# Optimization experiments

Measured on AMD Instinct MI355X. Metric: run time of the kernel, lower is better.

## Reference

```python
import jax, jax.numpy as jnp
import numpy as np

N = 100000   # node_size
R = 1000     # rel_size
T = 600000   # triple_size (edges)
D = 128      # node_dim
DEPTH = 2


def seg_softmax(logits, seg, num_segments):
    # softmax over irregular segments (rows of a sparse [N,N] matrix)
    m = jax.lax.stop_gradient(jax.ops.segment_max(logits, seg, num_segments=num_segments))
    e = jnp.exp(logits - m[seg])
    s = jax.ops.segment_sum(e, seg, num_segments=num_segments)
    return e / s[seg]


def setup_inputs() -> dict:
    key = jax.random.key(0)
    ks = jax.random.split(key, 10)
    xav = float(np.sqrt(6.0 / (D + 1)))
    features = jax.random.normal(ks[0], (N, D), dtype=jnp.float32)
    rel_emb = jax.random.normal(ks[1], (R, D), dtype=jnp.float32)
    # adj: (2, T) COO edges; rows sorted to mimic coalesced sparse tensor
    adj_row = jnp.sort(jax.random.randint(ks[2], (T,), 0, N))
    adj_col = jax.random.randint(ks[3], (T,), 0, N)
    adj = jnp.stack([adj_row, adj_col]).astype(jnp.int64)
    # r_index: (2, T) indices of sparse [T, R] matrix, one relation per triple
    r_index = jnp.stack([jnp.arange(T), jax.random.randint(ks[4], (T,), 0, R)]).astype(jnp.int64)
    r_val = jax.random.uniform(ks[5], (T,), dtype=jnp.float32)
    hn_row = jnp.sort(jax.random.randint(ks[6], (T,), 0, N))
    hn_col = jax.random.randint(ks[7], (T,), 0, N)
    high_nei = jnp.stack([hn_row, hn_col]).astype(jnp.int64)
    attn_kernels = jax.random.uniform(ks[8], (DEPTH, D, 1), jnp.float32, -xav, xav)
    high_atts = jax.random.uniform(ks[9], (DEPTH, D, 1), jnp.float32, -xav, xav)
    return {"features": features, "rel_emb": rel_emb, "r_val": r_val,
            "attn_kernels": attn_kernels, "high_atts": high_atts,
            "adj": adj, "r_index": r_index, "high_nei": high_nei}


def reference(features, rel_emb, r_val, attn_kernels, high_atts, adj, r_index, high_nei):
    row, col = adj[0], adj[1]
    hrow, hcol = high_nei[0], high_nei[1]
    outputs = []
    feats = jnp.tanh(features)
    outputs.append(feats)
    for l in range(DEPTH):
        # sparse [T,R] @ rel_emb -> per-triple relation embedding [T,D]
        tri_rel = jax.ops.segment_sum(r_val[:, None] * rel_emb[r_index[1]],
                                      r_index[0], num_segments=T)
        tri_rel = tri_rel / jnp.maximum(
            jnp.linalg.norm(tri_rel, axis=1, keepdims=True), 1e-12)
        neighs = feats[col]                                   # [T,D] gather
        # Householder reflection of neighbor features across tri_rel
        neighs = neighs - 2.0 * jnp.sum(neighs * tri_rel, axis=1, keepdims=True) * tri_rel
        att = (tri_rel @ attn_kernels[l])[:, 0]               # [T]
        att = seg_softmax(att, row, N)                        # sparse row softmax
        feats = jnp.tanh(jax.ops.segment_sum(neighs * att[:, None], row, num_segments=N))
        outputs.append(feats)
    for l in range(DEPTH):
        neighs = feats[hcol]                                  # [T,D]
        att = seg_softmax((neighs @ high_atts[l])[:, 0], hrow, N)
        feats = jnp.tanh(jax.ops.segment_sum(neighs * att[:, None], hrow, num_segments=N))
        outputs.append(feats)
    return jnp.concatenate(outputs, axis=-1)                  # [N, D*(2*DEPTH+1)]
```

## Files before the change

### kernel.cpp

```cpp
#include <hip/hip_runtime.h>
#include <math.h>

#define N_NODES 100000
#define R_REL   1000
#define T_TRI   600000
#define D_DIM   128
#define OUT_STRIDE 640

typedef unsigned int  u32;
typedef unsigned short u16;

__device__ __forceinline__ float wave_sum(float v) {
    #pragma unroll
    for (int off = 32; off > 0; off >>= 1) v += __shfl_xor(v, off);
    return v;
}
__device__ __forceinline__ float half32_sum(float v) {
    v += __shfl_xor(v, 1); v += __shfl_xor(v, 2); v += __shfl_xor(v, 4);
    v += __shfl_xor(v, 8); v += __shfl_xor(v, 16);
    return v;
}
__device__ __forceinline__ float sub16_sum(float v) {
    v += __shfl_xor(v, 1); v += __shfl_xor(v, 2);
    v += __shfl_xor(v, 4); v += __shfl_xor(v, 8);
    return v;
}
__device__ __forceinline__ float fast_tanh(float x) {
    float e = __expf(2.f * x);
    return 1.f - __fdividef(2.f, e + 1.f);
}
__device__ __forceinline__ float4 tanh4(float4 v) {
    float4 o; o.x = fast_tanh(v.x); o.y = fast_tanh(v.y);
    o.z = fast_tanh(v.z); o.w = fast_tanh(v.w);
    return o;
}
__device__ __forceinline__ float dot4(float4 a, float4 b) {
    return a.x*b.x + a.y*b.y + a.z*b.z + a.w*b.w;
}
__device__ __forceinline__ u32 bfr(float x) {
    u32 u = __float_as_uint(x);
    return (u + 0x7fffu + ((u >> 16) & 1u)) >> 16;
}
__device__ __forceinline__ uint2 pack_bf4(float4 v) {
    uint2 p;
    p.x = bfr(v.x) | (bfr(v.y) << 16);
    p.y = bfr(v.z) | (bfr(v.w) << 16);
    return p;
}
__device__ __forceinline__ void unpack_bf8(uint4 v, float f[8]) {
    f[0] = __uint_as_float(v.x << 16); f[1] = __uint_as_float(v.x & 0xffff0000u);
    f[2] = __uint_as_float(v.y << 16); f[3] = __uint_as_float(v.y & 0xffff0000u);
    f[4] = __uint_as_float(v.z << 16); f[5] = __uint_as_float(v.z & 0xffff0000u);
    f[6] = __uint_as_float(v.w << 16); f[7] = __uint_as_float(v.w & 0xffff0000u);
}

__global__ void k_tanh(const float* __restrict__ feat, float* __restrict__ out,
                       u16* __restrict__ bf0) {
    int i = blockIdx.x * blockDim.x + threadIdx.x;
    if (i >= N_NODES * D_DIM / 4) return;
    int n  = i / (D_DIM / 4);
    int d4 = i % (D_DIM / 4);
    float4 v = reinterpret_cast<const float4*>(feat)[i];
    float4 t = tanh4(v);
    reinterpret_cast<float4*>(out + (size_t)n * OUT_STRIDE)[d4] = t;
    reinterpret_cast<uint2*>(bf0 + (size_t)n * D_DIM)[d4] = pack_bf4(t);
}

__global__ void k_relprep(const float* __restrict__ rel, const float* __restrict__ attk,
                          float* __restrict__ wtab, float* __restrict__ fsc) {
    int r = blockIdx.x;
    int lane = threadIdx.x;
    float a0 = rel[r * D_DIM + lane], a1 = rel[r * D_DIM + 64 + lane];
    float nrm2 = wave_sum(a0 * a0 + a1 * a1);
    float d0  = wave_sum(a0 * attk[lane] + a1 * attk[64 + lane]);
    float d1  = wave_sum(a0 * attk[D_DIM + lane] + a1 * attk[D_DIM + 64 + lane]);
    if (lane == 0) {
        float inv = __frsqrt_rn(nrm2);
        wtab[r]         = __expf(d0 * inv);
        wtab[R_REL + r] = __expf(d1 * inv);
        fsc[r] = 2.f * inv * inv;
    }
}

__global__ void k_pack_rel(const float* __restrict__ rel, u16* __restrict__ relbf) {
    int t = blockIdx.x * blockDim.x + threadIdx.x;
    if (t >= R_REL * 16) return;
    int r = t >> 4, k = t & 15;
    const float4* src = (const float4*)(rel + (size_t)r * D_DIM + k * 8);
    uint2 pa = pack_bf4(src[0]), pb = pack_bf4(src[1]);
    uint4 o; o.x = pa.x; o.y = pa.y; o.z = pb.x; o.w = pb.y;
    ((uint4*)(relbf + (size_t)r * D_DIM))[k] = o;
}

__global__ void k_rowptr2(const int* __restrict__ rows_a, const int* __restrict__ rows_b,
                          int* __restrict__ pa, int* __restrict__ pb) {
    int i = blockIdx.x * blockDim.x + threadIdx.x;
    const int* rows; int* p; int n;
    if (i <= N_NODES) { rows = rows_a; p = pa; n = i; }
    else {
        n = i - (N_NODES + 1);
        if (n > N_NODES) return;
        rows = rows_b; p = pb;
    }
    int lo = 0, hi = T_TRI;
    while (lo < hi) { int mid = (lo + hi) >> 1; if (rows[mid] < n) lo = mid + 1; else hi = mid; }
    p[n] = lo;
}

__global__ __launch_bounds__(256) void k_nr_layer(
    float* __restrict__ outbuf, int out_off,
    const u16* __restrict__ in_bf,
    u16* __restrict__ out_bf,
    const int* __restrict__ row_ptr,
    const int* __restrict__ col,
    const int* __restrict__ ridx1,
    const float* __restrict__ r_val,
    const u16* __restrict__ rel_bf,
    const float* __restrict__ wtab,
    const float* __restrict__ fsc,
    const float* __restrict__ ha,
    float* __restrict__ eproj_out) {
    __shared__ float s_w[4][64];
    __shared__ float s_fs[4][64];
    int wslot = threadIdx.x >> 6;
    int lane  = threadIdx.x & 63;
    int wid2  = (blockIdx.x * blockDim.x + threadIdx.x) >> 6;
    int row   = wid2 * 2 + (lane >> 5);
    if (row >= N_NODES) return;
    int ll  = lane & 31;
    int sgl = (lane >> 4) & 1;
    int sl  = lane & 15;
    int beg = row_ptr[row], end = row_ptr[row + 1];
    int deg = end - beg;
    float* orow = outbuf + (size_t)row * OUT_STRIDE + out_off;

    if (deg == 0) {
        float4 z = {0.f,0.f,0.f,0.f};
        ((float4*)orow)[ll] = z;
        if (out_bf != nullptr && ll < 16) {
            uint4 zz = {0u,0u,0u,0u};
            ((uint4*)(out_bf + (size_t)row * D_DIM))[ll] = zz;
        }
        if (ha != nullptr && ll == 0) eproj_out[row] = 1.f;
        return;
    }

    int  t0 = beg + ll;
    bool va = t0 < end;
    int  ta = va ? t0 : beg;
    int  rt_a = ridx1[ta];
    float rv_a = r_val[ta];
    bool  z_a  = (rv_a == 0.f);
    float w_a  = z_a ? 1.f : wtab[rt_a];
    float fs_a = z_a ? 0.f : fsc[rt_a];
    w_a = va ? w_a : 0.f;

    int  tb0 = beg + sgl, tb1 = beg + 2 + sgl;
    bool v0 = tb0 < end, v1 = tb1 < end;
    int  tc0 = v0 ? tb0 : beg, tc1 = v1 ? tb1 : beg;
    int  cc0 = col[tc0],   cc1 = col[tc1];
    int  rr0 = ridx1[tc0], rr1 = ridx1[tc1];
    uint4 F0 = ((const uint4*)(in_bf  + (size_t)cc0 * D_DIM))[sl];
    uint4 R0 = ((const uint4*)(rel_bf + (size_t)rr0 * D_DIM))[sl];
    uint4 F1 = ((const uint4*)(in_bf  + (size_t)cc1 * D_DIM))[sl];
    uint4 R1 = ((const uint4*)(rel_bf + (size_t)rr1 * D_DIM))[sl];

    float lsum = w_a;
    for (int t = t0 + 32; t < end; t += 32) {
        int rt = ridx1[t]; float rv = r_val[t];
        lsum += (rv == 0.f) ? 1.f : wtab[rt];
    }
    float inv_s = 1.f / half32_sum(lsum);
    s_w[wslot][lane]  = w_a * inv_s;
    s_fs[wslot][lane] = fs_a;

    int hb = lane & 32;

    float w0  = v0 ? s_w[wslot][hb + sgl] : 0.f;
    float fs0 = s_fs[wslot][hb + sgl];
    float nf[8], rf[8];
    unpack_bf8(F0, nf); unpack_bf8(R0, rf);
    float pd = 0.f;
    #pragma unroll
    for (int j = 0; j < 8; ++j) pd += nf[j] * rf[j];
    pd = sub16_sum(pd);
    float f0 = fs0 * pd;
    float acc[8];
    #pragma unroll
    for (int j = 0; j < 8; ++j) acc[j] = w0 * (nf[j] - f0 * rf[j]);

    int niter = (deg + 1) >> 1;
    int cur_tc = tc1, cur_rr = rr1; bool cur_v = v1;
    for (int it = 1; it < niter; ++it) {
        int tb = beg + 2 * (it + 1) + sgl;
        bool nv = tb < end;
        int  ntc = nv ? tb : beg;
        int  ncc = col[ntc];
        int  nrr = ridx1[ntc];
        uint4 NF = ((const uint4*)(in_bf  + (size_t)ncc * D_DIM))[sl];
        uint4 NR = ((const uint4*)(rel_bf + (size_t)nrr * D_DIM))[sl];

        int idx = 2 * it + sgl;
        float w, fs;
        if (idx < 32) {
            w  = cur_v ? s_w[wslot][hb + idx] : 0.f;
            fs = s_fs[wslot][hb + idx];
        } else {
            float rv = r_val[cur_tc];
            bool z = (rv == 0.f);
            w  = cur_v ? (z ? 1.f : wtab[cur_rr]) * inv_s : 0.f;
            fs = z ? 0.f : fsc[cur_rr];
        }
        float gf[8], qf[8];
        unpack_bf8(F1, gf); unpack_bf8(R1, qf);
        float pdt = 0.f;
        #pragma unroll
        for (int j = 0; j < 8; ++j) pdt += gf[j] * qf[j];
        pdt = sub16_sum(pdt);
        float ft = fs * pdt;
        #pragma unroll
        for (int j = 0; j < 8; ++j) acc[j] += w * (gf[j] - ft * qf[j]);

        F1 = NF; R1 = NR;
        cur_tc = ntc; cur_rr = nrr; cur_v = nv;
    }

    #pragma unroll
    for (int j = 0; j < 8; ++j) acc[j] += __shfl_xor(acc[j], 16);

    float4 q = (sgl == 0) ? make_float4(acc[0], acc[1], acc[2], acc[3])
                          : make_float4(acc[4], acc[5], acc[6], acc[7]);
    float4 tq = tanh4(q);
    ((float4*)orow)[2 * sl + sgl] = tq;
    if (out_bf != nullptr)
        ((uint2*)(out_bf + (size_t)row * D_DIM))[2 * sl + sgl] = pack_bf4(tq);
    if (ha != nullptr) {
        const float4* ha4 = (const float4*)ha;
        float pdp = dot4(tq, ha4[2 * sl + sgl]);
        pdp = sub16_sum(pdp);
        pdp += __shfl_xor(pdp, 16);
        if (ll == 0) eproj_out[row] = __expf(pdp);
    }
}

__global__ __launch_bounds__(256) void k_high_layer(
    float* __restrict__ outbuf, int out_off,
    const u16* __restrict__ in_bf,
    u16* __restrict__ out_bf,
    const int* __restrict__ row_ptr,
    const int* __restrict__ hcol,
    const float* __restrict__ eproj,
    const float* __restrict__ ha,
    float* __restrict__ eproj_out) {
    __shared__ float s_w[4][64];
    int wslot = threadIdx.x >> 6;
    int lane  = threadIdx.x & 63;
    int wid2  = (blockIdx.x * blockDim.x + threadIdx.x) >> 6;
    int row   = wid2 * 2 + (lane >> 5);
    if (row >= N_NODES) return;
    int ll  = lane & 31;
    int sgl = (lane >> 4) & 1;
    int sl  = lane & 15;
    int beg = row_ptr[row], end = row_ptr[row + 1];
    int deg = end - beg;
    float* orow = outbuf + (size_t)row * OUT_STRIDE + out_off;

    if (deg == 0) {
        float4 z = {0.f,0.f,0.f,0.f};
        ((float4*)orow)[ll] = z;
        if (out_bf != nullptr && ll < 16) {
            uint4 zz = {0u,0u,0u,0u};
            ((uint4*)(out_bf + (size_t)row * D_DIM))[ll] = zz;
        }
        if (ha != nullptr && ll == 0) eproj_out[row] = 1.f;
        return;
    }

    int  t0 = beg + ll;
    bool va = t0 < end;
    int  ta = va ? t0 : beg;
    int  c_a = hcol[ta];
    float e_a = eproj[c_a];
    e_a = va ? e_a : 0.f;

    int  tb0 = beg + sgl, tb1 = beg + 2 + sgl;
    bool v0 = tb0 < end, v1 = tb1 < end;
    int  tc0 = v0 ? tb0 : beg, tc1 = v1 ? tb1 : beg;
    int  cc0 = hcol[tc0], cc1 = hcol[tc1];
    uint4 F0 = ((const uint4*)(in_bf + (size_t)cc0 * D_DIM))[sl];
    uint4 F1 = ((const uint4*)(in_bf + (size_t)cc1 * D_DIM))[sl];

    float lsum = e_a;
    for (int t = t0 + 32; t < end; t += 32)
        lsum += eproj[hcol[t]];
    float inv_s = 1.f / half32_sum(lsum);
    s_w[wslot][lane] = e_a * inv_s;

    int hb = lane & 32;

    float w0 = v0 ? s_w[wslot][hb + sgl] : 0.f;
    float nf[8];
    unpack_bf8(F0, nf);
    float acc[8];
    #pragma unroll
    for (int j = 0; j < 8; ++j) acc[j] = w0 * nf[j];

    int niter = (deg + 1) >> 1;
    int cur_cc = cc1; bool cur_v = v1;
    for (int it = 1; it < niter; ++it) {
        int tb = beg + 2 * (it + 1) + sgl;
        bool nv = tb < end;
        int  ntc = nv ? tb : beg;
        int  ncc = hcol[ntc];
        uint4 NF = ((const uint4*)(in_bf + (size_t)ncc * D_DIM))[sl];

        int idx = 2 * it + sgl;
        float w;
        if (idx < 32) w = cur_v ? s_w[wslot][hb + idx] : 0.f;
        else          w = cur_v ? eproj[cur_cc] * inv_s : 0.f;
        float gf[8];
        unpack_bf8(F1, gf);
        #pragma unroll
        for (int j = 0; j < 8; ++j) acc[j] += w * gf[j];

        F1 = NF; cur_cc = ncc; cur_v = nv;
    }

    #pragma unroll
    for (int j = 0; j < 8; ++j) acc[j] += __shfl_xor(acc[j], 16);

    float4 q = (sgl == 0) ? make_float4(acc[0], acc[1], acc[2], acc[3])
                          : make_float4(acc[4], acc[5], acc[6], acc[7]);
    float4 tq = tanh4(q);
    ((float4*)orow)[2 * sl + sgl] = tq;
    if (out_bf != nullptr)
        ((uint2*)(out_bf + (size_t)row * D_DIM))[2 * sl + sgl] = pack_bf4(tq);
    if (ha != nullptr) {
        const float4* ha4 = (const float4*)ha;
        float pdp = dot4(tq, ha4[2 * sl + sgl]);
        pdp = sub16_sum(pdp);
        pdp += __shfl_xor(pdp, 16);
        if (ll == 0) eproj_out[row] = __expf(pdp);
    }
}

extern "C" void kernel_launch(void* const* d_in, const int* in_sizes, int n_in,
                              void* d_out, int out_size, void* d_ws, size_t ws_size,
                              hipStream_t stream) {
    const float* features  = (const float*)d_in[0];
    const float* rel_emb   = (const float*)d_in[1];
    const float* r_val     = (const float*)d_in[2];
    const float* attk      = (const float*)d_in[3];
    const float* high_atts = (const float*)d_in[4];
    const int*   adj       = (const int*)d_in[5];
    const int*   r_index   = (const int*)d_in[6];
    const int*   high_nei  = (const int*)d_in[7];
    float* out = (float*)d_out;

    char* ws = (char*)d_ws;
    auto take = [&](size_t bytes) -> char* {
        char* p = ws;
        ws += (bytes + 255) & ~(size_t)255;
        return p;
    };
    int*   row_ptr_adj  = (int*)take((N_NODES + 1) * sizeof(int));
    int*   row_ptr_high = (int*)take((N_NODES + 1) * sizeof(int));
    float* wtab         = (float*)take(2 * R_REL * sizeof(float));
    float* fsc          = (float*)take(R_REL * sizeof(float));
    float* eproj0       = (float*)take(N_NODES * sizeof(float));
    float* eproj1       = (float*)take(N_NODES * sizeof(float));
    u16*   rel_bf       = (u16*)take((size_t)R_REL * D_DIM * sizeof(u16));
    u16*   fbf0         = (u16*)take((size_t)N_NODES * D_DIM * sizeof(u16));
    u16*   fbf1         = (u16*)take((size_t)N_NODES * D_DIM * sizeof(u16));
    u16*   fbf2         = (u16*)take((size_t)N_NODES * D_DIM * sizeof(u16));
    u16*   fbf3         = (u16*)take((size_t)N_NODES * D_DIM * sizeof(u16));

    k_tanh<<<(N_NODES * D_DIM / 4 + 255) / 256, 256, 0, stream>>>(features, out, fbf0);
    k_relprep<<<R_REL, 64, 0, stream>>>(rel_emb, attk, wtab, fsc);
    k_pack_rel<<<(R_REL * 16 + 255) / 256, 256, 0, stream>>>(rel_emb, rel_bf);
    k_rowptr2<<<(2 * (N_NODES + 1) + 255) / 256, 256, 0, stream>>>(
        adj, high_nei, row_ptr_adj, row_ptr_high);

    int pair_blocks = ((N_NODES + 1) / 2 + 3) / 4;

    k_nr_layer<<<pair_blocks, 256, 0, stream>>>(
        out, 1 * D_DIM, fbf0, fbf1,
        row_ptr_adj, adj + T_TRI, r_index + T_TRI, r_val,
        rel_bf, wtab + 0 * R_REL, fsc, nullptr, nullptr);
    k_nr_layer<<<pair_blocks, 256, 0, stream>>>(
        out, 2 * D_DIM, fbf1, fbf2,
        row_ptr_adj, adj + T_TRI, r_index + T_TRI, r_val,
        rel_bf, wtab + 1 * R_REL, fsc, high_atts + 0 * D_DIM, eproj0);
    k_high_layer<<<pair_blocks, 256, 0, stream>>>(
        out, 3 * D_DIM, fbf2, fbf3,
        row_ptr_high, high_nei + T_TRI, eproj0, high_atts + 1 * D_DIM, eproj1);
    k_high_layer<<<pair_blocks, 256, 0, stream>>>(
        out, 4 * D_DIM, fbf3, nullptr,
        row_ptr_high, high_nei + T_TRI, eproj1, nullptr, nullptr);
}
```

Baseline: 224.5 us.

## Sort rows by degree bucket and fuse prep kernels, prenormalize relation table

Merges the tanh, relation-prep, bf16 packing and row-pointer kernels into one grid-stride prep kernel. The same kernel builds a degree histogram, and two new kernels (scan and scatter) turn it into a degree-sorted row permutation. The layer kernels then process rows in that order so the two rows sharing a wave have similar degree, which cuts idle lanes. Relation embeddings are stored pre-normalized, which removes the per-relation scale table, and a sign bit in the shared weight marks zero-valued triples. The cost is extra launches, a second binary search per row, and scattered output writes because consecutive waves no longer handle consecutive rows.

```diff
diff --git a/kernel.cpp b/kernel.cpp
--- a/kernel.cpp
+++ b/kernel.cpp
@@ -6,6 +6,7 @@
 #define T_TRI   600000
 #define D_DIM   128
 #define OUT_STRIDE 640
+#define NBUCK   65
 
 typedef unsigned int  u32;
 typedef unsigned short u16;
@@ -54,57 +55,101 @@
     f[6] = __uint_as_float(v.w << 16); f[7] = __uint_as_float(v.w & 0xffff0000u);
 }
 
-__global__ void k_tanh(const float* __restrict__ feat, float* __restrict__ out,
-                       u16* __restrict__ bf0) {
-    int i = blockIdx.x * blockDim.x + threadIdx.x;
-    if (i >= N_NODES * D_DIM / 4) return;
-    int n  = i / (D_DIM / 4);
-    int d4 = i % (D_DIM / 4);
-    float4 v = reinterpret_cast<const float4*>(feat)[i];
-    float4 t = tanh4(v);
-    reinterpret_cast<float4*>(out + (size_t)n * OUT_STRIDE)[d4] = t;
-    reinterpret_cast<uint2*>(bf0 + (size_t)n * D_DIM)[d4] = pack_bf4(t);
-}
-
-__global__ void k_relprep(const float* __restrict__ rel, const float* __restrict__ attk,
-                          float* __restrict__ wtab, float* __restrict__ fsc) {
-    int r = blockIdx.x;
-    int lane = threadIdx.x;
-    float a0 = rel[r * D_DIM + lane], a1 = rel[r * D_DIM + 64 + lane];
-    float nrm2 = wave_sum(a0 * a0 + a1 * a1);
-    float d0  = wave_sum(a0 * attk[lane] + a1 * attk[64 + lane]);
-    float d1  = wave_sum(a0 * attk[D_DIM + lane] + a1 * attk[D_DIM + 64 + lane]);
-    if (lane == 0) {
+__global__ void k_prep(const float* __restrict__ feat, const float* __restrict__ rel,
+                       const float* __restrict__ attk,
+                       float* __restrict__ out, u16* __restrict__ bf0,
+                       u16* __restrict__ relu_bf, float* __restrict__ wtab,
+                       const int* __restrict__ adj_rows, const int* __restrict__ hn_rows,
+                       int* __restrict__ rpa, int* __restrict__ rph,
+                       u32* __restrict__ hist) {
+    __shared__ u32 lhist[2 * NBUCK];
+    int tid = threadIdx.x;
+    for (int i = tid; i < 2 * NBUCK; i += blockDim.x) lhist[i] = 0;
+    __syncthreads();
+    int gt = blockIdx.x * blockDim.x + tid;
+    int gstride = gridDim.x * blockDim.x;
+
+    for (int i = gt; i < N_NODES * D_DIM / 4; i += gstride) {
+        int n = i >> 5, d4 = i & 31;
+        float4 v = ((const float4*)feat)[i];
+        float4 t = tanh4(v);
+        ((float4*)(out + (size_t)n * OUT_STRIDE))[d4] = t;
+        ((uint2*)(bf0 + (size_t)n * D_DIM))[d4] = pack_bf4(t);
+    }
+    int gw = gt >> 6, lane = tid & 63;
+    int nwaves = gstride >> 6;
+    for (int r = gw; r < R_REL; r += nwaves) {
+        float2 a  = ((const float2*)rel)[r * 64 + lane];
+        float2 k0 = ((const float2*)attk)[lane];
+        float2 k1 = ((const float2*)(attk + D_DIM))[lane];
+        float nrm2 = wave_sum(a.x * a.x + a.y * a.y);
+        float d0 = wave_sum(a.x * k0.x + a.y * k0.y);
+        float d1 = wave_sum(a.x * k1.x + a.y * k1.y);
         float inv = __frsqrt_rn(nrm2);
-        wtab[r]         = __expf(d0 * inv);
-        wtab[R_REL + r] = __expf(d1 * inv);
-        fsc[r] = 2.f * inv * inv;
-    }
-}
-
-__global__ void k_pack_rel(const float* __restrict__ rel, u16* __restrict__ relbf) {
-    int t = blockIdx.x * blockDim.x + threadIdx.x;
-    if (t >= R_REL * 16) return;
-    int r = t >> 4, k = t & 15;
-    const float4* src = (const float4*)(rel + (size_t)r * D_DIM + k * 8);
-    uint2 pa = pack_bf4(src[0]), pb = pack_bf4(src[1]);
-    uint4 o; o.x = pa.x; o.y = pa.y; o.z = pb.x; o.w = pb.y;
-    ((uint4*)(relbf + (size_t)r * D_DIM))[k] = o;
-}
-
-__global__ void k_rowptr2(const int* __restrict__ rows_a, const int* __restrict__ rows_b,
-                          int* __restrict__ pa, int* __restrict__ pb) {
-    int i = blockIdx.x * blockDim.x + threadIdx.x;
-    const int* rows; int* p; int n;
-    if (i <= N_NODES) { rows = rows_a; p = pa; n = i; }
-    else {
-        n = i - (N_NODES + 1);
-        if (n > N_NODES) return;
-        rows = rows_b; p = pb;
-    }
-    int lo = 0, hi = T_TRI;
-    while (lo < hi) { int mid = (lo + hi) >> 1; if (rows[mid] < n) lo = mid + 1; else hi = mid; }
-    p[n] = lo;
+        ((u32*)relu_bf)[r * 64 + lane] = bfr(a.x * inv) | (bfr(a.y * inv) << 16);
+        if (lane == 0) {
+            wtab[r]         = __expf(d0 * inv);
+            wtab[R_REL + r] = __expf(d1 * inv);
+        }
+    }
+    for (int i = gt; i < 2 * (N_NODES + 1); i += gstride) {
+        const int* rows; int* p; int n;
+        if (i <= N_NODES) { rows = adj_rows; p = rpa; n = i; }
+        else { rows = hn_rows; p = rph; n = i - (N_NODES + 1); }
+        int lo = 0, hi = T_TRI;
+        while (lo < hi) { int m = (lo + hi) >> 1; if (rows[m] < n) lo = m + 1; else hi = m; }
+        p[n] = lo;
+    }
+    for (int i = gt; i < 2 * N_NODES; i += gstride) {
+        const int* rows = (i < N_NODES) ? adj_rows : hn_rows;
+        int n = (i < N_NODES) ? i : i - N_NODES;
+        int lo = 0, hi = T_TRI;
+        while (lo < hi) { int m = (lo + hi) >> 1; if (rows[m] < n) lo = m + 1; else hi = m; }
+        int lo2 = lo, hi2 = T_TRI;
+        while (lo2 < hi2) { int m = (lo2 + hi2) >> 1; if (rows[m] < n + 1) lo2 = m + 1; else hi2 = m; }
+        int b = min(lo2 - lo, 64);
+        atomicAdd(&lhist[((i < N_NODES) ? 0 : NBUCK) + b], 1u);
+    }
+    __syncthreads();
+    for (int i = tid; i < 2 * NBUCK; i += blockDim.x)
+        if (lhist[i]) atomicAdd(&hist[i], lhist[i]);
+}
+
+__global__ void k_scan(const u32* __restrict__ hist, u32* __restrict__ goff) {
+    if (threadIdx.x == 0 && blockIdx.x == 0) {
+        u32 s = 0;
+        for (int b = 0; b < NBUCK; ++b) { goff[b] = s; s += hist[b]; }
+        s = 0;
+        for (int b = 0; b < NBUCK; ++b) { goff[NBUCK + b] = s; s += hist[NBUCK + b]; }
+    }
+}
+
+__global__ void k_scatter(const int* __restrict__ rpa, const int* __restrict__ rph,
+                          u32* __restrict__ goff,
+                          int* __restrict__ perm_adj, int* __restrict__ perm_high) {
+    __shared__ u32 lcnt[2 * NBUCK];
+    __shared__ u32 lbase[2 * NBUCK];
+    __shared__ u32 lpos[2 * NBUCK];
+    int tid = threadIdx.x;
+    for (int i = tid; i < 2 * NBUCK; i += blockDim.x) { lcnt[i] = 0; lpos[i] = 0; }
+    __syncthreads();
+    int gt = blockIdx.x * blockDim.x + tid;
+    int b = -1, n = -1;
+    if (gt < 2 * N_NODES) {
+        const int* rp = (gt < N_NODES) ? rpa : rph;
+        n = (gt < N_NODES) ? gt : gt - N_NODES;
+        int deg = rp[n + 1] - rp[n];
+        b = min(deg, 64) + ((gt < N_NODES) ? 0 : NBUCK);
+        atomicAdd(&lcnt[b], 1u);
+    }
+    __syncthreads();
+    for (int i = tid; i < 2 * NBUCK; i += blockDim.x)
+        if (lcnt[i]) lbase[i] = atomicAdd(&goff[i], lcnt[i]);
+    __syncthreads();
+    if (b >= 0) {
+        u32 pos = lbase[b] + atomicAdd(&lpos[b], 1u);
+        if (b < NBUCK) perm_adj[pos] = n; else perm_high[pos] = n;
+    }
 }
 
 __global__ __launch_bounds__(256) void k_nr_layer(
@@ -115,18 +160,18 @@
     const int* __restrict__ col,
     const int* __restrict__ ridx1,
     const float* __restrict__ r_val,
-    const u16* __restrict__ rel_bf,
+    const u16* __restrict__ relu_bf,
     const float* __restrict__ wtab,
-    const float* __restrict__ fsc,
+    const int* __restrict__ perm,
     const float* __restrict__ ha,
     float* __restrict__ eproj_out) {
     __shared__ float s_w[4][64];
-    __shared__ float s_fs[4][64];
     int wslot = threadIdx.x >> 6;
     int lane  = threadIdx.x & 63;
     int wid2  = (blockIdx.x * blockDim.x + threadIdx.x) >> 6;
-    int row   = wid2 * 2 + (lane >> 5);
-    if (row >= N_NODES) return;
+    int idx2  = wid2 * 2 + (lane >> 5);
+    if (idx2 >= N_NODES) return;
+    int row = perm[idx2];
     int ll  = lane & 31;
     int sgl = (lane >> 4) & 1;
     int sl  = lane & 15;
@@ -151,19 +196,17 @@
     int  rt_a = ridx1[ta];
     float rv_a = r_val[ta];
     bool  z_a  = (rv_a == 0.f);
-    float w_a  = z_a ? 1.f : wtab[rt_a];
-    float fs_a = z_a ? 0.f : fsc[rt_a];
-    w_a = va ? w_a : 0.f;
+    float w_a  = va ? (z_a ? 1.f : wtab[rt_a]) : 0.f;
 
     int  tb0 = beg + sgl, tb1 = beg + 2 + sgl;
     bool v0 = tb0 < end, v1 = tb1 < end;
     int  tc0 = v0 ? tb0 : beg, tc1 = v1 ? tb1 : beg;
     int  cc0 = col[tc0],   cc1 = col[tc1];
     int  rr0 = ridx1[tc0], rr1 = ridx1[tc1];
-    uint4 F0 = ((const uint4*)(in_bf  + (size_t)cc0 * D_DIM))[sl];
-    uint4 R0 = ((const uint4*)(rel_bf + (size_t)rr0 * D_DIM))[sl];
-    uint4 F1 = ((const uint4*)(in_bf  + (size_t)cc1 * D_DIM))[sl];
-    uint4 R1 = ((const uint4*)(rel_bf + (size_t)rr1 * D_DIM))[sl];
+    uint4 F0 = ((const uint4*)(in_bf   + (size_t)cc0 * D_DIM))[sl];
+    uint4 U0 = ((const uint4*)(relu_bf + (size_t)rr0 * D_DIM))[sl];
+    uint4 F1 = ((const uint4*)(in_bf   + (size_t)cc1 * D_DIM))[sl];
+    uint4 U1 = ((const uint4*)(relu_bf + (size_t)rr1 * D_DIM))[sl];
 
     float lsum = w_a;
     for (int t = t0 + 32; t < end; t += 32) {
@@ -171,23 +214,22 @@
         lsum += (rv == 0.f) ? 1.f : wtab[rt];
     }
     float inv_s = 1.f / half32_sum(lsum);
-    s_w[wslot][lane]  = w_a * inv_s;
-    s_fs[wslot][lane] = fs_a;
-
+    float sw = w_a * inv_s;
+    s_w[wslot][lane] = z_a ? -sw : sw;
     int hb = lane & 32;
 
-    float w0  = v0 ? s_w[wslot][hb + sgl] : 0.f;
-    float fs0 = s_fs[wslot][hb + sgl];
-    float nf[8], rf[8];
-    unpack_bf8(F0, nf); unpack_bf8(R0, rf);
+    float sv = s_w[wslot][hb + sgl];
+    float w0 = fabsf(sv);
+    float nf[8], uf[8];
+    unpack_bf8(F0, nf); unpack_bf8(U0, uf);
     float pd = 0.f;
     #pragma unroll
-    for (int j = 0; j < 8; ++j) pd += nf[j] * rf[j];
+    for (int j = 0; j < 8; ++j) pd += nf[j] * uf[j];
     pd = sub16_sum(pd);
-    float f0 = fs0 * pd;
+    float b0 = (sv < 0.f) ? 0.f : 2.f * w0 * pd;
     float acc[8];
     #pragma unroll
-    for (int j = 0; j < 8; ++j) acc[j] = w0 * (nf[j] - f0 * rf[j]);
+    for (int j = 0; j < 8; ++j) acc[j] = w0 * nf[j] - b0 * uf[j];
 
     int niter = (deg + 1) >> 1;
     int cur_tc = tc1, cur_rr = rr1; bool cur_v = v1;
@@ -197,31 +239,30 @@
         int  ntc = nv ? tb : beg;
         int  ncc = col[ntc];
         int  nrr = ridx1[ntc];
-        uint4 NF = ((const uint4*)(in_bf  + (size_t)ncc * D_DIM))[sl];
-        uint4 NR = ((const uint4*)(rel_bf + (size_t)nrr * D_DIM))[sl];
+        uint4 NF = ((const uint4*)(in_bf   + (size_t)ncc * D_DIM))[sl];
+        uint4 NU = ((const uint4*)(relu_bf + (size_t)nrr * D_DIM))[sl];
 
         int idx = 2 * it + sgl;
-        float w, fs;
-        if (idx < 32) {
-            w  = cur_v ? s_w[wslot][hb + idx] : 0.f;
-            fs = s_fs[wslot][hb + idx];
-        } else {
+        float sv2;
+        if (idx < 32) sv2 = s_w[wslot][hb + idx];
+        else {
             float rv = r_val[cur_tc];
             bool z = (rv == 0.f);
-            w  = cur_v ? (z ? 1.f : wtab[cur_rr]) * inv_s : 0.f;
-            fs = z ? 0.f : fsc[cur_rr];
+            float wv = cur_v ? (z ? 1.f : wtab[cur_rr]) * inv_s : 0.f;
+            sv2 = z ? -wv : wv;
         }
+        float w = fabsf(sv2);
         float gf[8], qf[8];
-        unpack_bf8(F1, gf); unpack_bf8(R1, qf);
+        unpack_bf8(F1, gf); unpack_bf8(U1, qf);
         float pdt = 0.f;
         #pragma unroll
         for (int j = 0; j < 8; ++j) pdt += gf[j] * qf[j];
         pdt = sub16_sum(pdt);
-        float ft = fs * pdt;
+        float bt = (sv2 < 0.f) ? 0.f : 2.f * w * pdt;
         #pragma unroll
-        for (int j = 0; j < 8; ++j) acc[j] += w * (gf[j] - ft * qf[j]);
-
-        F1 = NF; R1 = NR;
+        for (int j = 0; j < 8; ++j) acc[j] += w * gf[j] - bt * qf[j];
+
+        F1 = NF; U1 = NU;
         cur_tc = ntc; cur_rr = nrr; cur_v = nv;
     }
 
@@ -250,14 +291,16 @@
     const int* __restrict__ row_ptr,
     const int* __restrict__ hcol,
     const float* __restrict__ eproj,
+    const int* __restrict__ perm,
     const float* __restrict__ ha,
     float* __restrict__ eproj_out) {
     __shared__ float s_w[4][64];
     int wslot = threadIdx.x >> 6;
     int lane  = threadIdx.x & 63;
     int wid2  = (blockIdx.x * blockDim.x + threadIdx.x) >> 6;
-    int row   = wid2 * 2 + (lane >> 5);
-    if (row >= N_NODES) return;
+    int idx2  = wid2 * 2 + (lane >> 5);
+    if (idx2 >= N_NODES) return;
+    int row = perm[idx2];
     int ll  = lane & 31;
     int sgl = (lane >> 4) & 1;
     int sl  = lane & 15;
@@ -295,10 +338,9 @@
         lsum += eproj[hcol[t]];
     float inv_s = 1.f / half32_sum(lsum);
     s_w[wslot][lane] = e_a * inv_s;
-
     int hb = lane & 32;
 
-    float w0 = v0 ? s_w[wslot][hb + sgl] : 0.f;
+    float w0 = s_w[wslot][hb + sgl];
     float nf[8];
     unpack_bf8(F0, nf);
     float acc[8];
@@ -316,7 +358,7 @@
 
         int idx = 2 * it + sgl;
         float w;
-        if (idx < 32) w = cur_v ? s_w[wslot][hb + idx] : 0.f;
+        if (idx < 32) w = s_w[wslot][hb + idx];
         else          w = cur_v ? eproj[cur_cc] * inv_s : 0.f;
         float gf[8];
         unpack_bf8(F1, gf);
@@ -363,38 +405,46 @@
         ws += (bytes + 255) & ~(size_t)255;
         return p;
     };
+    u32*   hist         = (u32*)take(2 * NBUCK * sizeof(u32));
+    u32*   goff         = (u32*)take(2 * NBUCK * sizeof(u32));
     int*   row_ptr_adj  = (int*)take((N_NODES + 1) * sizeof(int));
     int*   row_ptr_high = (int*)take((N_NODES + 1) * sizeof(int));
+    int*   perm_adj     = (int*)take(N_NODES * sizeof(int));
+    int*   perm_high    = (int*)take(N_NODES * sizeof(int));
     float* wtab         = (float*)take(2 * R_REL * sizeof(float));
-    float* fsc          = (float*)take(R_REL * sizeof(float));
     float* eproj0       = (float*)take(N_NODES * sizeof(float));
     float* eproj1       = (float*)take(N_NODES * sizeof(float));
-    u16*   rel_bf       = (u16*)take((size_t)R_REL * D_DIM * sizeof(u16));
+    u16*   relu_bf      = (u16*)take((size_t)R_REL * D_DIM * sizeof(u16));
     u16*   fbf0         = (u16*)take((size_t)N_NODES * D_DIM * sizeof(u16));
     u16*   fbf1         = (u16*)take((size_t)N_NODES * D_DIM * sizeof(u16));
     u16*   fbf2         = (u16*)take((size_t)N_NODES * D_DIM * sizeof(u16));
     u16*   fbf3         = (u16*)take((size_t)N_NODES * D_DIM * sizeof(u16));
 
-    k_tanh<<<(N_NODES * D_DIM / 4 + 255) / 256, 256, 0, stream>>>(features, out, fbf0);
-    k_relprep<<<R_REL, 64, 0, stream>>>(rel_emb, attk, wtab, fsc);
-    k_pack_rel<<<(R_REL * 16 + 255) / 256, 256, 0, stream>>>(rel_emb, rel_bf);
-    k_rowptr2<<<(2 * (N_NODES + 1) + 255) / 256, 256, 0, stream>>>(
-        adj, high_nei, row_ptr_adj, row_ptr_high);
+    hipMemsetAsync(hist, 0, 2 * 256 + 2 * NBUCK * sizeof(u32), stream);
+
+    k_prep<<<4096, 256, 0, stream>>>(features, rel_emb, attk, out, fbf0,
+                                     relu_bf, wtab, adj, high_nei,
+                                     row_ptr_adj, row_ptr_high, hist);
+    k_scan<<<1, 64, 0, stream>>>(hist, goff);
+    k_scatter<<<(2 * N_NODES + 255) / 256, 256, 0, stream>>>(
+        row_ptr_adj, row_ptr_high, goff, perm_adj, perm_high);
 
     int pair_blocks = ((N_NODES + 1) / 2 + 3) / 4;
 
     k_nr_layer<<<pair_blocks, 256, 0, stream>>>(
         out, 1 * D_DIM, fbf0, fbf1,
         row_ptr_adj, adj + T_TRI, r_index + T_TRI, r_val,
-        rel_bf, wtab + 0 * R_REL, fsc, nullptr, nullptr);
+        relu_bf, wtab + 0 * R_REL, perm_adj, nullptr, nullptr);
     k_nr_layer<<<pair_blocks, 256, 0, stream>>>(
         out, 2 * D_DIM, fbf1, fbf2,
         row_ptr_adj, adj + T_TRI, r_index + T_TRI, r_val,
-        rel_bf, wtab + 1 * R_REL, fsc, high_atts + 0 * D_DIM, eproj0);
+        relu_bf, wtab + 1 * R_REL, perm_adj, high_atts + 0 * D_DIM, eproj0);
     k_high_layer<<<pair_blocks, 256, 0, stream>>>(
         out, 3 * D_DIM, fbf2, fbf3,
-        row_ptr_high, high_nei + T_TRI, eproj0, high_atts + 1 * D_DIM, eproj1);
+        row_ptr_high, high_nei + T_TRI, eproj0, perm_high,
+        high_atts + 1 * D_DIM, eproj1);
     k_high_layer<<<pair_blocks, 256, 0, stream>>>(
         out, 4 * D_DIM, fbf3, nullptr,
-        row_ptr_high, high_nei + T_TRI, eproj1, nullptr, nullptr);
-}
+        row_ptr_high, high_nei + T_TRI, eproj1, perm_high,
+        nullptr, nullptr);
+}
```

New measurement: 236.1 us. +5.2%, slower.
